# Kernel optimization log

Hardware: AMD Instinct MI355X
Metric: run time of the kernel (lower is better)

The kernel has to match this reference:

```python
import jax, jax.numpy as jnp
import numpy as np

B, S_IMG, S_TXT, P, D, HEADS, HD = 1, 2048, 512, 4, 3072, 24, 128


def rmsnorm(x, weight=None, eps=1e-6):
    var = jnp.mean(jnp.square(x), axis=-1, keepdims=True)
    y = x * jax.lax.rsqrt(var + eps)
    return y * weight if weight is not None else y


def apply_rope(x, cos, sin):
    # x: [B,H,S,Dh]; cos/sin: [S,Dh]; interleaved real/imag rotation (diffusers use_real_unbind_dim=-1)
    xr = x.reshape(*x.shape[:-1], -1, 2)
    rot = jnp.stack([-xr[..., 1], xr[..., 0]], axis=-1).reshape(x.shape)
    return x * cos[None, None] + rot * sin[None, None]


def sdpa(q, k, v):
    scores = jnp.einsum('bhqd,bhkd->bhqk', q, k) / jnp.sqrt(jnp.asarray(q.shape[-1], q.dtype))
    return jnp.einsum('bhqk,bhkd->bhqd', jax.nn.softmax(scores, axis=-1), v)


def heads_split(x):
    # [B,S,D] -> [B,H,S,Dh]
    return x.reshape(x.shape[0], x.shape[1], HEADS, HD).transpose(0, 2, 1, 3)


def heads_merge(x):
    # [B,H,S,Dh] -> [B,S,D]
    return x.transpose(0, 2, 1, 3).reshape(x.shape[0], x.shape[2], HEADS * HD)


def setup_inputs() -> dict:
    key = jax.random.key(0)
    ks = jax.random.split(key, 32)
    init = lambda k, shape: (jax.random.normal(k, shape, dtype=jnp.float32) * 0.02)
    inp = {
        'hidden_states': jax.random.normal(ks[0], (B, S_IMG, D), dtype=jnp.float32),
        'encoder_hidden_states': jax.random.normal(ks[1], (B, S_TXT, D), dtype=jnp.float32),
        'ip_encoder_hidden_states': jax.random.normal(ks[2], (B, P, D), dtype=jnp.float32),
        'layer_scale': jax.random.uniform(ks[3], (B,), dtype=jnp.float32),
        'Wq': init(ks[4], (D, D)), 'bq': jnp.zeros((D,), jnp.float32),
        'Wk': init(ks[5], (D, D)), 'bk': jnp.zeros((D,), jnp.float32),
        'Wv': init(ks[6], (D, D)), 'bv': jnp.zeros((D,), jnp.float32),
        'norm_q_w': jnp.ones((HD,), jnp.float32),
        'norm_k_w': jnp.ones((HD,), jnp.float32),
        'Waq': init(ks[7], (D, D)), 'baq': jnp.zeros((D,), jnp.float32),
        'Wak': init(ks[8], (D, D)), 'bak': jnp.zeros((D,), jnp.float32),
        'Wav': init(ks[9], (D, D)), 'bav': jnp.zeros((D,), jnp.float32),
        'norm_aq_w': jnp.ones((HD,), jnp.float32),
        'norm_ak_w': jnp.ones((HD,), jnp.float32),
        'Wk_ip': init(ks[10], (D, D)),
        'Wv_ip': init(ks[11], (D, D)),
        'Wo': init(ks[12], (D, D)), 'bo': jnp.zeros((D,), jnp.float32),
        'Wao': init(ks[13], (D, D)), 'bao': jnp.zeros((D,), jnp.float32),
    }
    # rotary cos/sin over the joint (text+image) sequence, interleaved freqs per diffusers FLUX
    pos = jnp.arange(S_TXT + S_IMG, dtype=jnp.float32)
    inv_freq = 1.0 / (10000.0 ** (jnp.arange(0, HD, 2, dtype=jnp.float32) / HD))
    angles = pos[:, None] * inv_freq[None, :]            # [S, HD/2]
    angles = jnp.repeat(angles, 2, axis=-1)              # [S, HD]
    inp['cos'] = jnp.cos(angles)
    inp['sin'] = jnp.sin(angles)
    return inp


IP_SCALE = 1.0  # self.scale


def reference(hidden_states, encoder_hidden_states, ip_encoder_hidden_states, cos, sin,
              layer_scale, Wq, bq, Wk, bk, Wv, bv, norm_q_w, norm_k_w,
              Waq, baq, Wak, bak, Wav, bav, norm_aq_w, norm_ak_w,
              Wk_ip, Wv_ip, Wo, bo, Wao, bao):
    # image-stream projections
    q = heads_split(hidden_states @ Wq.T + bq)
    k = heads_split(hidden_states @ Wk.T + bk)
    v = heads_split(hidden_states @ Wv.T + bv)
    q = rmsnorm(q, norm_q_w, 1e-6)
    k = rmsnorm(k, norm_k_w, 1e-6)

    # IP-adapter cross-attention (queries = image tokens, kv = IP tokens)
    ip_k = rmsnorm(heads_split(ip_encoder_hidden_states @ Wk_ip.T), None, 1e-5)
    ip_v = heads_split(ip_encoder_hidden_states @ Wv_ip.T)
    ip_out = heads_merge(sdpa(q, ip_k, ip_v))            # [B, S_img, D]

    # text (encoder) stream projections, prepended to joint sequence
    eq = rmsnorm(heads_split(encoder_hidden_states @ Waq.T + baq), norm_aq_w, 1e-6)
    ek = rmsnorm(heads_split(encoder_hidden_states @ Wak.T + bak), norm_ak_w, 1e-6)
    ev = heads_split(encoder_hidden_states @ Wav.T + bav)
    q = jnp.concatenate([eq, q], axis=2)
    k = jnp.concatenate([ek, k], axis=2)
    v = jnp.concatenate([ev, v], axis=2)

    q = apply_rope(q, cos, sin)
    k = apply_rope(k, cos, sin)

    out = heads_merge(sdpa(q, k, v))                     # [B, S_txt+S_img, D]
    n_txt = encoder_hidden_states.shape[1]
    enc_out, img_out = out[:, :n_txt], out[:, n_txt:]

    ls = layer_scale.reshape(-1, 1, 1)
    img_out = img_out + IP_SCALE * ls * ip_out
    img_out = img_out @ Wo.T + bo
    enc_out = enc_out @ Wao.T + bao
    return (img_out, enc_out)
```

## Files before the change

### kernel.cpp

```cpp
#include <hip/hip_runtime.h>

typedef _Float16 half_t;
typedef _Float16 half2v __attribute__((ext_vector_type(2)));
typedef _Float16 half4v __attribute__((ext_vector_type(4)));
typedef _Float16 half8v __attribute__((ext_vector_type(8)));
typedef float    float4v __attribute__((ext_vector_type(4)));
typedef short    short8v __attribute__((ext_vector_type(8)));

#define S_IMG 2048
#define S_TXT 512
#define S_TOT 2560
#define NH    24
#define HD    128
#define DM    3072

__device__ __forceinline__ void gload16(const void* g, void* l) {
  __builtin_amdgcn_global_load_lds(
      (const __attribute__((address_space(1))) unsigned int*)g,
      (__attribute__((address_space(3))) unsigned int*)l, 16, 0, 0);
}

__global__ void cvt_kernel(const float* __restrict__ s, half_t* __restrict__ d, int n) {
  int i = (blockIdx.x * 256 + threadIdx.x) * 4;
  int stride = gridDim.x * 256 * 4;
  for (; i < n; i += stride) {
    float4v v = *(const float4v*)(s + i);
    half4v h;
    h[0] = (half_t)v[0]; h[1] = (half_t)v[1]; h[2] = (half_t)v[2]; h[3] = (half_t)v[3];
    *(half4v*)(d + i) = h;
  }
}

__global__ void cvt3_kernel(const float* __restrict__ s0, const float* __restrict__ s1,
                            const float* __restrict__ s2,
                            half_t* __restrict__ d0, half_t* __restrict__ d1,
                            half_t* __restrict__ d2, int n) {
  const float* s = blockIdx.y == 0 ? s0 : (blockIdx.y == 1 ? s1 : s2);
  half_t* d = blockIdx.y == 0 ? d0 : (blockIdx.y == 1 ? d1 : d2);
  int i = (blockIdx.x * 256 + threadIdx.x) * 8;
  int stride = gridDim.x * 256 * 8;
  for (; i < n; i += stride) {
    float4v v0 = *(const float4v*)(s + i);
    float4v v1 = *(const float4v*)(s + i + 4);
    half8v h;
    h[0] = (half_t)v0[0]; h[1] = (half_t)v0[1]; h[2] = (half_t)v0[2]; h[3] = (half_t)v0[3];
    h[4] = (half_t)v1[0]; h[5] = (half_t)v1[1]; h[6] = (half_t)v1[2]; h[7] = (half_t)v1[3];
    *(half8v*)(d + i) = h;
  }
}

template <typename OUT>
__device__ __forceinline__ void gemm_tile(half_t* As, half_t* Bs,
                                          const half_t* __restrict__ A,
                                          const half_t* __restrict__ Bt,
                                          const float* __restrict__ bias,
                                          OUT* __restrict__ C, int bm, int bn) {
  const int K = DM, N = DM;
  const int tid = threadIdx.x, wid = tid >> 6, l = tid & 63;
  const int wm = (wid >> 1) * 64, wn = (wid & 1) * 64;
  const int l15 = l & 15, l4 = l >> 4;
  float4v acc[4][4] = {};

  const int scol = ((l & 3) ^ ((l >> 3) & 3)) * 8;
  const half_t* ga = A + (long)(bm + wid * 32 + (l >> 2)) * K + scol;
  const half_t* gb = Bt + (long)(bn + wid * 32 + (l >> 2)) * K + scol;
  const long rowstep = 16l * K;

#define GSTAGE(T, SEL)                                                        \
  {                                                                           \
    char* a_d = (char*)As + (SEL) * 8192 + wid * 2048;                        \
    char* b_d = (char*)Bs + (SEL) * 8192 + wid * 2048;                        \
    int k0 = (T) * 32;                                                        \
    gload16(ga + k0, a_d);                                                    \
    gload16(ga + rowstep + k0, a_d + 1024);                                   \
    gload16(gb + k0, b_d);                                                    \
    gload16(gb + rowstep + k0, b_d + 1024);                                   \
  }

  GSTAGE(0, 0);
  GSTAGE(1, 1);

  const int NT = K / 32;
  const int cofs = (l4 * 16) ^ (((l15 >> 1) & 3) << 4);
  for (int t = 0; t < NT; t++) {
    int cur = t % 3;
    if (t + 1 < NT) asm volatile("s_waitcnt vmcnt(4)" ::: "memory");
    else            asm volatile("s_waitcnt vmcnt(0)" ::: "memory");
    __builtin_amdgcn_s_barrier();
    __builtin_amdgcn_sched_barrier(0);
    if (t + 2 < NT) GSTAGE(t + 2, (t + 2) % 3);
    __builtin_amdgcn_sched_barrier(0);
    const char* AsB = (const char*)As + cur * 8192;
    const char* BsB = (const char*)Bs + cur * 8192;
    half8v af[4], bf[4];
#pragma unroll
    for (int i = 0; i < 4; i++)
      af[i] = *(const half8v*)(AsB + (wm + i * 16 + l15) * 64 + cofs);
#pragma unroll
    for (int j = 0; j < 4; j++)
      bf[j] = *(const half8v*)(BsB + (wn + j * 16 + l15) * 64 + cofs);
    __builtin_amdgcn_s_setprio(1);
#pragma unroll
    for (int i = 0; i < 4; i++)
#pragma unroll
      for (int j = 0; j < 4; j++)
        acc[i][j] = __builtin_amdgcn_mfma_f32_16x16x32_f16(af[i], bf[j], acc[i][j], 0, 0, 0);
    __builtin_amdgcn_s_setprio(0);
  }
#undef GSTAGE
#pragma unroll
  for (int i = 0; i < 4; i++)
#pragma unroll
    for (int j = 0; j < 4; j++) {
      int row = bm + wm + i * 16 + l4 * 4;
      int col = bn + wn + j * 16 + l15;
      float bv = bias ? bias[col] : 0.0f;
#pragma unroll
      for (int r = 0; r < 4; r++) {
        float v = acc[i][j][r] + bv;
        C[(long)(row + r) * N + col] = (OUT)v;
      }
    }
}

template <int NROW>
__global__ __launch_bounds__(256) void gemm3_kernel(const half_t* __restrict__ A,
                                                    const half_t* __restrict__ W0,
                                                    const half_t* __restrict__ W1,
                                                    const half_t* __restrict__ W2,
                                                    const float* b0, const float* b1, const float* b2,
                                                    half_t* O0, half_t* O1, half_t* O2) {
  __shared__ half_t As[3 * 128 * 32];
  __shared__ half_t Bs[3 * 128 * 32];
  int b = blockIdx.x;
  int q = (72 * NROW) >> 3;
  int wg = (b & 7) * q + (b >> 3);
  int col = wg / NROW, row = wg % NROW;
  int sel = col / 24;
  const half_t* Bt = sel == 0 ? W0 : (sel == 1 ? W1 : W2);
  const float* bias = sel == 0 ? b0 : (sel == 1 ? b1 : b2);
  half_t* C = sel == 0 ? O0 : (sel == 1 ? O1 : O2);
  gemm_tile<half_t>(As, Bs, A, Bt, bias, C, row * 128, (col % 24) * 128);
}

__global__ __launch_bounds__(256) void gemm_out_kernel(const half_t* __restrict__ ocomb,
                                                       const half_t* __restrict__ Wo_h,
                                                       const half_t* __restrict__ Wao_h,
                                                       const float* bo, const float* bao,
                                                       float* out_img, float* out_enc) {
  __shared__ half_t As[3 * 128 * 32];
  __shared__ half_t Bs[3 * 128 * 32];
  int b = blockIdx.x;
  int wg = (b & 7) * 60 + (b >> 3);
  int col = wg / 20, r = wg % 20;
  bool enc = r >= 16;
  const half_t* A = enc ? ocomb : ocomb + (long)S_TXT * DM;
  int bm = (enc ? (r - 16) : r) * 128;
  gemm_tile<float>(As, Bs, A, enc ? Wao_h : Wo_h, enc ? bao : bo,
                   enc ? out_enc : out_img, bm, col * 128);
}

__global__ __launch_bounds__(256) void ip_proj_kernel(const float* __restrict__ x,
                                                      const float* __restrict__ W,
                                                      float* __restrict__ out) {
  int n = blockIdx.x * 4 + (threadIdx.x >> 6);
  int l = threadIdx.x & 63;
  const float* wr = W + (long)n * DM;
  float acc[4] = {0.f, 0.f, 0.f, 0.f};
  for (int k = l * 4; k < DM; k += 256) {
    float4v wv = *(const float4v*)(wr + k);
#pragma unroll
    for (int p = 0; p < 4; p++) {
      float4v xv = *(const float4v*)(x + p * DM + k);
      acc[p] += wv[0] * xv[0] + wv[1] * xv[1] + wv[2] * xv[2] + wv[3] * xv[3];
    }
  }
#pragma unroll
  for (int off = 32; off; off >>= 1)
#pragma unroll
    for (int p = 0; p < 4; p++) acc[p] += __shfl_xor(acc[p], off, 64);
  if (l == 0)
#pragma unroll
    for (int p = 0; p < 4; p++) out[p * DM + n] = acc[p];
}

__global__ void ip_norm_kernel(const float* __restrict__ kr, const float* __restrict__ vr,
                               half_t* __restrict__ kh, half_t* __restrict__ vh) {
  int t = blockIdx.x;
  int l = threadIdx.x;
  int d = l * 2;
  if (t < 96) {
    int base = (t / 24) * DM + (t % 24) * HD;
    float x0 = kr[base + d], x1 = kr[base + d + 1];
    float ss = x0 * x0 + x1 * x1;
#pragma unroll
    for (int off = 32; off; off >>= 1) ss += __shfl_xor(ss, off, 64);
    float r = rsqrtf(ss * (1.0f / HD) + 1e-5f);
    kh[base + d] = (half_t)(x0 * r);
    kh[base + d + 1] = (half_t)(x1 * r);
  } else {
    int t2 = t - 96;
    int base = (t2 / 24) * DM + (t2 % 24) * HD;
    vh[base + d] = (half_t)vr[base + d];
    vh[base + d + 1] = (half_t)vr[base + d + 1];
  }
}

__global__ __launch_bounds__(256) void prep_kernel(
    const half_t* __restrict__ qraw, const half_t* __restrict__ kraw,
    const half_t* __restrict__ eq, const half_t* __restrict__ ek,
    const float* __restrict__ nqw, const float* __restrict__ nkw,
    const float* __restrict__ naqw, const float* __restrict__ nakw,
    const float* __restrict__ cosb, const float* __restrict__ sinb,
    half_t* __restrict__ qcat, half_t* __restrict__ kcat, half_t* __restrict__ qnr) {
  int task = blockIdx.x * 4 + (threadIdx.x >> 6);
  int l = threadIdx.x & 63;
  int s = task / NH, h = task - (task / NH) * NH;
  int d = l * 2;
  const half_t *qs, *ks;
  const float *wq, *wk;
  if (s < S_TXT) {
    long base = (long)s * DM + h * HD;
    qs = eq + base; ks = ek + base;
    wq = naqw; wk = nakw;
  } else {
    long base = (long)(s - S_TXT) * DM + h * HD;
    qs = qraw + base; ks = kraw + base;
    wq = nqw; wk = nkw;
  }
  half2v qv = *(const half2v*)(qs + d);
  half2v kv = *(const half2v*)(ks + d);
  float q0 = (float)qv[0], q1 = (float)qv[1];
  float k0 = (float)kv[0], k1 = (float)kv[1];
  float ssq = q0 * q0 + q1 * q1;
  float ssk = k0 * k0 + k1 * k1;
#pragma unroll
  for (int off = 32; off; off >>= 1) {
    ssq += __shfl_xor(ssq, off, 64);
    ssk += __shfl_xor(ssk, off, 64);
  }
  float rq = rsqrtf(ssq * (1.0f / HD) + 1e-6f);
  float rk = rsqrtf(ssk * (1.0f / HD) + 1e-6f);
  float qn0 = q0 * rq * wq[d], qn1 = q1 * rq * wq[d + 1];
  float kn0 = k0 * rk * wk[d], kn1 = k1 * rk * wk[d + 1];
  if (s >= S_TXT) {
    half2v o; o[0] = (half_t)qn0; o[1] = (half_t)qn1;
    *(half2v*)(qnr + ((long)h * S_IMG + (s - S_TXT)) * HD + d) = o;
  }
  float c0 = cosb[s * HD + d], c1 = cosb[s * HD + d + 1];
  float s0 = sinb[s * HD + d], s1 = sinb[s * HD + d + 1];
  float qo0 = qn0 * c0 - qn1 * s0, qo1 = qn1 * c1 + qn0 * s1;
  float ko0 = kn0 * c0 - kn1 * s0, ko1 = kn1 * c1 + kn0 * s1;
  long ci = ((long)h * S_TOT + s) * HD + d;
  half2v oq; oq[0] = (half_t)qo0; oq[1] = (half_t)qo1;
  half2v ok; ok[0] = (half_t)ko0; ok[1] = (half_t)ko1;
  *(half2v*)(qcat + ci) = oq;
  *(half2v*)(kcat + ci) = ok;
}

__global__ __launch_bounds__(256) void vtrans_kernel(const half_t* __restrict__ ev,
                                                     const half_t* __restrict__ vraw,
                                                     half_t* __restrict__ vcatT) {
  __shared__ half_t T[64][136];
  int h = blockIdx.y, sb = blockIdx.x * 64;
  int t = threadIdx.x;
#pragma unroll
  for (int i = 0; i < 4; i++) {
    int c = t + i * 256;
    int row = c >> 4, col = (c & 15) * 8;
    int s = sb + row;
    const half_t* src = (s < S_TXT) ? ev + (long)s * DM + h * HD + col
                                    : vraw + (long)(s - S_TXT) * DM + h * HD + col;
    *(half8v*)&T[row][col] = *(const half8v*)src;
  }
  __syncthreads();
#pragma unroll
  for (int i = 0; i < 4; i++) {
    int c = t + i * 256;
    int d = c >> 3, sc = (c & 7) * 8;
    half8v v;
#pragma unroll
    for (int j = 0; j < 8; j++) v[j] = T[sc + j][d];
    *(half8v*)(vcatT + ((long)h * HD + d) * S_TOT + sb + sc) = v;
  }
}

__global__ __launch_bounds__(256) void ip_attn_kernel(const half_t* __restrict__ qnr,
                                                      const half_t* __restrict__ kh,
                                                      const half_t* __restrict__ vh,
                                                      half_t* __restrict__ ipout) {
  int tid = threadIdx.x;
  int task = blockIdx.x * 16 + (tid >> 4);
  int l16 = tid & 15;
  int h = task >> 11;
  int s = task & 2047;
  int d = l16 * 8;
  half8v qv = *(const half8v*)(qnr + ((long)h * S_IMG + s) * HD + d);
  float sc[4];
#pragma unroll
  for (int p = 0; p < 4; p++) {
    half8v kv = *(const half8v*)(kh + p * DM + h * HD + d);
    float a = 0.f;
#pragma unroll
    for (int j = 0; j < 8; j++) a += (float)qv[j] * (float)kv[j];
    sc[p] = a;
  }
#pragma unroll
  for (int off = 8; off; off >>= 1)
#pragma unroll
    for (int p = 0; p < 4; p++) sc[p] += __shfl_xor(sc[p], off, 16);
  float m = fmaxf(fmaxf(sc[0], sc[1]), fmaxf(sc[2], sc[3]));
  float e[4], sum = 0.f;
#pragma unroll
  for (int p = 0; p < 4; p++) { e[p] = __expf((sc[p] - m) * 0.088388347648318447f); sum += e[p]; }
  float inv = 1.0f / sum;
  float o[8] = {};
#pragma unroll
  for (int p = 0; p < 4; p++) {
    half8v vv = *(const half8v*)(vh + p * DM + h * HD + d);
#pragma unroll
    for (int j = 0; j < 8; j++) o[j] += e[p] * (float)vv[j];
  }
  half8v ov;
#pragma unroll
  for (int j = 0; j < 8; j++) ov[j] = (half_t)(o[j] * inv);
  *(half8v*)(ipout + (long)s * DM + h * HD + d) = ov;
}

__global__ __launch_bounds__(256, 2) void flash_kernel(const half_t* __restrict__ qcat,
                                                       const half_t* __restrict__ kcat,
                                                       const half_t* __restrict__ vcatT,
                                                       const half_t* __restrict__ ipout,
                                                       const float* __restrict__ lsp,
                                                       half_t* __restrict__ ocomb) {
  __shared__ half_t Ks[3 * 32 * 128];
  __shared__ half_t Vs[3 * 128 * 32];
  __shared__ half_t Pw[4][32 * 40];
  int b = blockIdx.x;
  int wg = (b & 7) * 60 + (b >> 3);
  const int h = wg / 20, qb = wg % 20;
  const int tid = threadIdx.x, wid = tid >> 6, l = tid & 63;
  const int l15 = l & 15, l4 = l >> 4;
  const float CEXP = 0.12754137969983614f;

  half8v qf[2][4];
#pragma unroll
  for (int t = 0; t < 2; t++) {
    int qrow = qb * 128 + wid * 32 + t * 16 + l15;
    const half_t* qp = qcat + ((long)h * S_TOT + qrow) * HD;
#pragma unroll
    for (int kk = 0; kk < 4; kk++) qf[t][kk] = *(const half8v*)(qp + kk * 32 + l4 * 8);
  }
  float4v o[2][8] = {};
  float mreg[2] = {-3.0e38f, -3.0e38f};
  float lreg[2] = {0.f, 0.f};
  const float ls = lsp[0];

  const char* kb = (const char*)(kcat + (long)h * S_TOT * HD);
  const char* vb = (const char*)(vcatT + (long)h * HD * S_TOT);
  int kof[2];
  long vof[2];
#pragma unroll
  for (int c = 0; c < 2; c++) {
    int L = wid * 2048 + c * 1024 + l * 16;
    kof[c] = L ^ (((L >> 8) & 7) << 4);
    int vrow = L >> 6;
    vof[c] = (long)vrow * (S_TOT * 2) + ((L & 63) ^ (((vrow >> 1) & 3) << 4));
  }

#define STAGE(KT, SEL)                                                        \
  {                                                                           \
    char* kd = (char*)Ks + (SEL) * 8192 + wid * 2048;                         \
    char* vd = (char*)Vs + (SEL) * 8192 + wid * 2048;                         \
    _Pragma("unroll") for (int c = 0; c < 2; c++) {                           \
      gload16(kb + (long)(KT) * 256 + kof[c], kd + c * 1024);                 \
      gload16(vb + vof[c] + (KT) * 2, vd + c * 1024);                         \
    }                                                                         \
  }

  STAGE(0, 0);
  STAGE(32, 1);

  const int NT = S_TOT / 32;
  const int vofs = (l4 * 16) ^ (((l15 >> 1) & 3) << 4);
  for (int it = 0; it < NT; it++) {
    int cur = it % 3;
    if (it + 1 < NT) asm volatile("s_waitcnt vmcnt(4)" ::: "memory");
    else             asm volatile("s_waitcnt vmcnt(0)" ::: "memory");
    __builtin_amdgcn_s_barrier();
    __builtin_amdgcn_sched_barrier(0);
    if (it + 2 < NT) STAGE((it + 2) * 32, (it + 2) % 3);

    const char* KsB = (const char*)Ks + cur * 8192;
    const char* VsB = (const char*)Vs + cur * 8192;

    float4v s0[2] = {}, s1[2] = {};
    __builtin_amdgcn_s_setprio(1);
#pragma unroll
    for (int nb = 0; nb < 2; nb++) {
      int krow = nb * 16 + l15;
      int rb = krow << 8;
      int sw = (krow & 7) << 4;
#pragma unroll
      for (int kk = 0; kk < 4; kk++) {
        half8v kf = *(const half8v*)(KsB + rb + ((kk * 64 + l4 * 16) ^ sw));
        s0[nb] = __builtin_amdgcn_mfma_f32_16x16x32_f16(kf, qf[0][kk], s0[nb], 0, 0, 0);
        s1[nb] = __builtin_amdgcn_mfma_f32_16x16x32_f16(kf, qf[1][kk], s1[nb], 0, 0, 0);
      }
    }
    __builtin_amdgcn_s_setprio(0);
#pragma unroll
    for (int t = 0; t < 2; t++) {
      float4v* st = t ? s1 : s0;
      float mt = fmaxf(fmaxf(fmaxf(st[0][0], st[0][1]), fmaxf(st[0][2], st[0][3])),
                       fmaxf(fmaxf(st[1][0], st[1][1]), fmaxf(st[1][2], st[1][3])));
      mt = fmaxf(mt, __shfl_xor(mt, 16, 64));
      mt = fmaxf(mt, __shfl_xor(mt, 32, 64));
      if (__any((mt - mreg[t]) * CEXP > 8.0f)) {
        float mn = fmaxf(mreg[t], mt);
        float alv = exp2f((mreg[t] - mn) * CEXP);
        mreg[t] = mn;
        lreg[t] *= alv;
#pragma unroll
        for (int r = 0; r < 4; r++) {
          float ar = __shfl(alv, l4 * 4 + r, 64);
#pragma unroll
          for (int cb = 0; cb < 8; cb++) o[t][cb][r] *= ar;
        }
      }
      float sum = 0.f;
#pragma unroll
      for (int nb = 0; nb < 2; nb++) {
        half4v ph;
#pragma unroll
        for (int r = 0; r < 4; r++) {
          float e = exp2f((st[nb][r] - mreg[t]) * CEXP);
          sum += e;
          ph[r] = (half_t)e;
        }
        *(half4v*)&Pw[wid][(t * 16 + l15) * 40 + nb * 16 + l4 * 4] = ph;
      }
      sum += __shfl_xor(sum, 16, 64);
      sum += __shfl_xor(sum, 32, 64);
      lreg[t] += sum;
    }
    half8v pa0 = *(const half8v*)&Pw[wid][l15 * 40 + l4 * 8];
    half8v pa1 = *(const half8v*)&Pw[wid][(16 + l15) * 40 + l4 * 8];
    __builtin_amdgcn_s_setprio(1);
#pragma unroll
    for (int cb = 0; cb < 8; cb++) {
      int row = cb * 16 + l15;
      half8v vf = *(const half8v*)(VsB + row * 64 + vofs);
      o[0][cb] = __builtin_amdgcn_mfma_f32_16x16x32_f16(pa0, vf, o[0][cb], 0, 0, 0);
      o[1][cb] = __builtin_amdgcn_mfma_f32_16x16x32_f16(pa1, vf, o[1][cb], 0, 0, 0);
    }
    __builtin_amdgcn_s_setprio(0);
  }
#undef STAGE
#pragma unroll
  for (int t = 0; t < 2; t++) {
    float invq = 1.0f / lreg[t];
#pragma unroll
    for (int r = 0; r < 4; r++) {
      float inv = __shfl(invq, l4 * 4 + r, 64);
      int s = qb * 128 + wid * 32 + t * 16 + l4 * 4 + r;
#pragma unroll
      for (int cb = 0; cb < 8; cb++) {
        int col = h * HD + cb * 16 + l15;
        float val = o[t][cb][r] * inv;
        if (s >= S_TXT) val += ls * (float)ipout[(long)(s - S_TXT) * DM + col];
        ocomb[(long)s * DM + col] = (half_t)val;
      }
    }
  }
}

extern "C" void kernel_launch(void* const* d_in, const int* in_sizes, int n_in,
                              void* d_out, int out_size, void* d_ws, size_t ws_size,
                              hipStream_t stream) {
  (void)in_sizes; (void)n_in; (void)out_size; (void)ws_size;
  const float* hs    = (const float*)d_in[0];
  const float* enc   = (const float*)d_in[1];
  const float* ipenc = (const float*)d_in[2];
  const float* lsc   = (const float*)d_in[3];
  const float* Wq  = (const float*)d_in[4];  const float* bq  = (const float*)d_in[5];
  const float* Wk  = (const float*)d_in[6];  const float* bk  = (const float*)d_in[7];
  const float* Wv  = (const float*)d_in[8];  const float* bv  = (const float*)d_in[9];
  const float* nqw = (const float*)d_in[10]; const float* nkw = (const float*)d_in[11];
  const float* Waq = (const float*)d_in[12]; const float* baq = (const float*)d_in[13];
  const float* Wak = (const float*)d_in[14]; const float* bak = (const float*)d_in[15];
  const float* Wav = (const float*)d_in[16]; const float* bav = (const float*)d_in[17];
  const float* naqw= (const float*)d_in[18]; const float* nakw= (const float*)d_in[19];
  const float* Wkip= (const float*)d_in[20]; const float* Wvip= (const float*)d_in[21];
  const float* Wo  = (const float*)d_in[22]; const float* bo  = (const float*)d_in[23];
  const float* Wao = (const float*)d_in[24]; const float* bao = (const float*)d_in[25];
  const float* cosb= (const float*)d_in[26]; const float* sinb= (const float*)d_in[27];

  const size_t WSZ = (size_t)DM * DM;
  const size_t HSZ = (size_t)S_IMG * DM;
  const size_t ESZ = (size_t)S_TXT * DM;
  const size_t CSZ = (size_t)NH * S_TOT * HD;

  half_t* base = (half_t*)d_ws;
  half_t* W3    = base;
  half_t* hs_h  = W3 + 3 * WSZ;
  half_t* enc_h = hs_h + HSZ;
  half_t* qkvr  = enc_h + ESZ;
  half_t* eqkv  = qkvr + 3 * HSZ;
  half_t* qcat  = eqkv + 3 * ESZ;
  half_t* kcat  = qcat + CSZ;
  half_t* vcatT = kcat + CSZ;

  half_t* q_raw = qkvr;
  half_t* k_raw = qkvr + HSZ;
  half_t* v_raw = qkvr + 2 * HSZ;
  half_t* eq_r  = eqkv;
  half_t* ek_r  = eqkv + ESZ;
  half_t* ev_r  = eqkv + 2 * ESZ;
  half_t* qnr   = hs_h;
  half_t* ipout = qkvr;
  half_t* ocomb = qkvr + HSZ;
  float*  ipk_raw = (float*)enc_h;
  float*  ipv_raw = ipk_raw + 4 * DM;
  half_t* ipk_h  = enc_h + 16 * DM;
  half_t* ipv_h  = ipk_h + 4 * DM;

  cvt_kernel<<<1024, 256, 0, stream>>>(hs, hs_h, (int)HSZ);
  cvt_kernel<<<512, 256, 0, stream>>>(enc, enc_h, (int)ESZ);

  cvt3_kernel<<<dim3(1024, 3), 256, 0, stream>>>(Wq, Wk, Wv, W3, W3 + WSZ, W3 + 2 * WSZ, (int)WSZ);
  gemm3_kernel<16><<<1152, 256, 0, stream>>>(hs_h, W3, W3 + WSZ, W3 + 2 * WSZ,
                                             bq, bk, bv, q_raw, k_raw, v_raw);
  cvt3_kernel<<<dim3(1024, 3), 256, 0, stream>>>(Waq, Wak, Wav, W3, W3 + WSZ, W3 + 2 * WSZ, (int)WSZ);
  gemm3_kernel<4><<<288, 256, 0, stream>>>(enc_h, W3, W3 + WSZ, W3 + 2 * WSZ,
                                           baq, bak, bav, eq_r, ek_r, ev_r);
  ip_proj_kernel<<<768, 256, 0, stream>>>(ipenc, Wkip, ipk_raw);
  ip_proj_kernel<<<768, 256, 0, stream>>>(ipenc, Wvip, ipv_raw);
  ip_norm_kernel<<<192, 64, 0, stream>>>(ipk_raw, ipv_raw, ipk_h, ipv_h);

  prep_kernel<<<(S_TOT * NH) / 4, 256, 0, stream>>>(q_raw, k_raw, eq_r, ek_r,
                                                    nqw, nkw, naqw, nakw, cosb, sinb,
                                                    qcat, kcat, qnr);
  vtrans_kernel<<<dim3(S_TOT / 64, NH), 256, 0, stream>>>(ev_r, v_raw, vcatT);

  ip_attn_kernel<<<(NH * S_IMG) / 16, 256, 0, stream>>>(qnr, ipk_h, ipv_h, ipout);

  flash_kernel<<<480, 256, 0, stream>>>(qcat, kcat, vcatT, ipout, lsc, ocomb);

  float* out_img = (float*)d_out;
  float* out_enc = (float*)d_out + (size_t)S_IMG * DM;
  cvt3_kernel<<<dim3(1024, 2), 256, 0, stream>>>(Wo, Wao, Wao, W3, W3 + WSZ, W3 + 2 * WSZ, (int)WSZ);
  gemm_out_kernel<<<480, 256, 0, stream>>>(ocomb, W3, W3 + WSZ, bo, bao, out_img, out_enc);
}
```

Measured before the change: 600.0 us.

## Enlarge GEMM tiles to 128x256 with 8 waves, widen flash KV tile, merge launches

The GEMM tile grows to 128x256 with 512 threads (8 waves), which halves the grid and raises B-tile reuse per A load. The flash attention kernel now processes 64-key tiles with double buffering instead of 32-key triple buffering, and does the PV MFMA per query sub-tile. The activation conversions and the two IP projections are each merged into a single launch. The larger tiles reduce the number of workgroups, and the change of buffering may expose load latency or lower occupancy.

Result: slower. 642.7 us (+7.1%).

```diff
diff --git a/kernel.cpp b/kernel.cpp
--- a/kernel.cpp
+++ b/kernel.cpp
@@ -20,14 +20,20 @@
       (__attribute__((address_space(3))) unsigned int*)l, 16, 0, 0);
 }
 
-__global__ void cvt_kernel(const float* __restrict__ s, half_t* __restrict__ d, int n) {
-  int i = (blockIdx.x * 256 + threadIdx.x) * 4;
-  int stride = gridDim.x * 256 * 4;
-  for (; i < n; i += stride) {
-    float4v v = *(const float4v*)(s + i);
-    half4v h;
-    h[0] = (half_t)v[0]; h[1] = (half_t)v[1]; h[2] = (half_t)v[2]; h[3] = (half_t)v[3];
-    *(half4v*)(d + i) = h;
+__global__ void cvt_act_kernel(const float* __restrict__ hs, const float* __restrict__ enc,
+                               half_t* __restrict__ d) {
+  const long NHS = (long)S_IMG * DM;
+  const long TOT = NHS + (long)S_TXT * DM;
+  long i = ((long)blockIdx.x * 256 + threadIdx.x) * 8;
+  long stride = (long)gridDim.x * 256 * 8;
+  for (; i < TOT; i += stride) {
+    const float* s = i < NHS ? hs + i : enc + (i - NHS);
+    float4v v0 = *(const float4v*)(s);
+    float4v v1 = *(const float4v*)(s + 4);
+    half8v h;
+    h[0] = (half_t)v0[0]; h[1] = (half_t)v0[1]; h[2] = (half_t)v0[2]; h[3] = (half_t)v0[3];
+    h[4] = (half_t)v1[0]; h[5] = (half_t)v1[1]; h[6] = (half_t)v1[2]; h[7] = (half_t)v1[3];
+    *(half8v*)(d + i) = h;
   }
 }
 
@@ -57,24 +63,23 @@
                                           OUT* __restrict__ C, int bm, int bn) {
   const int K = DM, N = DM;
   const int tid = threadIdx.x, wid = tid >> 6, l = tid & 63;
-  const int wm = (wid >> 1) * 64, wn = (wid & 1) * 64;
+  const int wm = (wid >> 2) * 64, wn = (wid & 3) * 64;
   const int l15 = l & 15, l4 = l >> 4;
   float4v acc[4][4] = {};
 
-  const int scol = ((l & 3) ^ ((l >> 3) & 3)) * 8;
-  const half_t* ga = A + (long)(bm + wid * 32 + (l >> 2)) * K + scol;
-  const half_t* gb = Bt + (long)(bn + wid * 32 + (l >> 2)) * K + scol;
-  const long rowstep = 16l * K;
+  const int scol = ((tid & 3) ^ ((tid >> 3) & 3)) * 8;
+  const half_t* ga = A + (long)(bm + (tid >> 2)) * K + scol;
+  const half_t* gb = Bt + (long)(bn + (tid >> 2)) * K + scol;
+  const long rowstepB = 128l * K;
 
 #define GSTAGE(T, SEL)                                                        \
   {                                                                           \
-    char* a_d = (char*)As + (SEL) * 8192 + wid * 2048;                        \
-    char* b_d = (char*)Bs + (SEL) * 8192 + wid * 2048;                        \
+    char* a_d = (char*)As + (SEL) * 8192 + wid * 1024;                        \
+    char* b_d = (char*)Bs + (SEL) * 16384 + wid * 1024;                       \
     int k0 = (T) * 32;                                                        \
     gload16(ga + k0, a_d);                                                    \
-    gload16(ga + rowstep + k0, a_d + 1024);                                   \
     gload16(gb + k0, b_d);                                                    \
-    gload16(gb + rowstep + k0, b_d + 1024);                                   \
+    gload16(gb + rowstepB + k0, b_d + 8192);                                  \
   }
 
   GSTAGE(0, 0);
@@ -84,14 +89,14 @@
   const int cofs = (l4 * 16) ^ (((l15 >> 1) & 3) << 4);
   for (int t = 0; t < NT; t++) {
     int cur = t % 3;
-    if (t + 1 < NT) asm volatile("s_waitcnt vmcnt(4)" ::: "memory");
+    if (t + 1 < NT) asm volatile("s_waitcnt vmcnt(3)" ::: "memory");
     else            asm volatile("s_waitcnt vmcnt(0)" ::: "memory");
     __builtin_amdgcn_s_barrier();
     __builtin_amdgcn_sched_barrier(0);
     if (t + 2 < NT) GSTAGE(t + 2, (t + 2) % 3);
     __builtin_amdgcn_sched_barrier(0);
     const char* AsB = (const char*)As + cur * 8192;
-    const char* BsB = (const char*)Bs + cur * 8192;
+    const char* BsB = (const char*)Bs + cur * 16384;
     half8v af[4], bf[4];
 #pragma unroll
     for (int i = 0; i < 4; i++)
@@ -124,45 +129,49 @@
 }
 
 template <int NROW>
-__global__ __launch_bounds__(256) void gemm3_kernel(const half_t* __restrict__ A,
-                                                    const half_t* __restrict__ W0,
-                                                    const half_t* __restrict__ W1,
-                                                    const half_t* __restrict__ W2,
-                                                    const float* b0, const float* b1, const float* b2,
-                                                    half_t* O0, half_t* O1, half_t* O2) {
-  __shared__ half_t As[3 * 128 * 32];
-  __shared__ half_t Bs[3 * 128 * 32];
+__global__ __launch_bounds__(512, 4) void gemm3_kernel(const half_t* __restrict__ A,
+                                                       const half_t* __restrict__ W0,
+                                                       const half_t* __restrict__ W1,
+                                                       const half_t* __restrict__ W2,
+                                                       const float* b0, const float* b1, const float* b2,
+                                                       half_t* O0, half_t* O1, half_t* O2) {
+  __shared__ half_t As[3 * 4096];
+  __shared__ half_t Bs[3 * 8192];
   int b = blockIdx.x;
-  int q = (72 * NROW) >> 3;
+  int q = (36 * NROW) >> 3;
   int wg = (b & 7) * q + (b >> 3);
   int col = wg / NROW, row = wg % NROW;
-  int sel = col / 24;
+  int sel = col / 12;
   const half_t* Bt = sel == 0 ? W0 : (sel == 1 ? W1 : W2);
   const float* bias = sel == 0 ? b0 : (sel == 1 ? b1 : b2);
   half_t* C = sel == 0 ? O0 : (sel == 1 ? O1 : O2);
-  gemm_tile<half_t>(As, Bs, A, Bt, bias, C, row * 128, (col % 24) * 128);
-}
-
-__global__ __launch_bounds__(256) void gemm_out_kernel(const half_t* __restrict__ ocomb,
-                                                       const half_t* __restrict__ Wo_h,
-                                                       const half_t* __restrict__ Wao_h,
-                                                       const float* bo, const float* bao,
-                                                       float* out_img, float* out_enc) {
-  __shared__ half_t As[3 * 128 * 32];
-  __shared__ half_t Bs[3 * 128 * 32];
+  gemm_tile<half_t>(As, Bs, A, Bt, bias, C, row * 128, (col % 12) * 256);
+}
+
+__global__ __launch_bounds__(512, 4) void gemm_out_kernel(const half_t* __restrict__ ocomb,
+                                                          const half_t* __restrict__ Wo_h,
+                                                          const half_t* __restrict__ Wao_h,
+                                                          const float* bo, const float* bao,
+                                                          float* out_img, float* out_enc) {
+  __shared__ half_t As[3 * 4096];
+  __shared__ half_t Bs[3 * 8192];
   int b = blockIdx.x;
-  int wg = (b & 7) * 60 + (b >> 3);
+  int wg = (b & 7) * 30 + (b >> 3);
   int col = wg / 20, r = wg % 20;
   bool enc = r >= 16;
   const half_t* A = enc ? ocomb : ocomb + (long)S_TXT * DM;
   int bm = (enc ? (r - 16) : r) * 128;
   gemm_tile<float>(As, Bs, A, enc ? Wao_h : Wo_h, enc ? bao : bo,
-                   enc ? out_enc : out_img, bm, col * 128);
+                   enc ? out_enc : out_img, bm, col * 256);
 }
 
 __global__ __launch_bounds__(256) void ip_proj_kernel(const float* __restrict__ x,
-                                                      const float* __restrict__ W,
-                                                      float* __restrict__ out) {
+                                                      const float* __restrict__ Wk_ip,
+                                                      const float* __restrict__ Wv_ip,
+                                                      float* __restrict__ outk,
+                                                      float* __restrict__ outv) {
+  const float* W = blockIdx.y ? Wv_ip : Wk_ip;
+  float* out = blockIdx.y ? outv : outk;
   int n = blockIdx.x * 4 + (threadIdx.x >> 6);
   int l = threadIdx.x & 63;
   const float* wr = W + (long)n * DM;
@@ -333,9 +342,9 @@
                                                        const half_t* __restrict__ ipout,
                                                        const float* __restrict__ lsp,
                                                        half_t* __restrict__ ocomb) {
-  __shared__ half_t Ks[3 * 32 * 128];
-  __shared__ half_t Vs[3 * 128 * 32];
-  __shared__ half_t Pw[4][32 * 40];
+  __shared__ half_t Ks[2 * 64 * 128];
+  __shared__ half_t Vs[2 * 128 * 64];
+  __shared__ half_t Pw[4][16 * 72];
   int b = blockIdx.x;
   int wg = (b & 7) * 60 + (b >> 3);
   const int h = wg / 20, qb = wg % 20;
@@ -358,46 +367,43 @@
 
   const char* kb = (const char*)(kcat + (long)h * S_TOT * HD);
   const char* vb = (const char*)(vcatT + (long)h * HD * S_TOT);
-  int kof[2];
-  long vof[2];
-#pragma unroll
-  for (int c = 0; c < 2; c++) {
-    int L = wid * 2048 + c * 1024 + l * 16;
+  int kof[4];
+  long vof[4];
+#pragma unroll
+  for (int c = 0; c < 4; c++) {
+    int L = c * 4096 + tid * 16;
     kof[c] = L ^ (((L >> 8) & 7) << 4);
-    int vrow = L >> 6;
-    vof[c] = (long)vrow * (S_TOT * 2) + ((L & 63) ^ (((vrow >> 1) & 3) << 4));
+    int vrow = L >> 7;
+    vof[c] = (long)vrow * (S_TOT * 2) + ((L & 127) ^ ((vrow & 7) << 4));
   }
 
 #define STAGE(KT, SEL)                                                        \
   {                                                                           \
-    char* kd = (char*)Ks + (SEL) * 8192 + wid * 2048;                         \
-    char* vd = (char*)Vs + (SEL) * 8192 + wid * 2048;                         \
-    _Pragma("unroll") for (int c = 0; c < 2; c++) {                           \
-      gload16(kb + (long)(KT) * 256 + kof[c], kd + c * 1024);                 \
-      gload16(vb + vof[c] + (KT) * 2, vd + c * 1024);                         \
+    char* kd = (char*)Ks + (SEL) * 16384 + wid * 1024;                        \
+    char* vd = (char*)Vs + (SEL) * 16384 + wid * 1024;                        \
+    _Pragma("unroll") for (int c = 0; c < 4; c++) {                           \
+      gload16(kb + (long)(KT) * 256 + kof[c], kd + c * 4096);                 \
+      gload16(vb + vof[c] + (KT) * 2, vd + c * 4096);                         \
     }                                                                         \
   }
 
   STAGE(0, 0);
-  STAGE(32, 1);
-
-  const int NT = S_TOT / 32;
-  const int vofs = (l4 * 16) ^ (((l15 >> 1) & 3) << 4);
+
+  const int NT = S_TOT / 64;
+  int sel = 0;
   for (int it = 0; it < NT; it++) {
-    int cur = it % 3;
-    if (it + 1 < NT) asm volatile("s_waitcnt vmcnt(4)" ::: "memory");
-    else             asm volatile("s_waitcnt vmcnt(0)" ::: "memory");
+    asm volatile("s_waitcnt vmcnt(0)" ::: "memory");
     __builtin_amdgcn_s_barrier();
     __builtin_amdgcn_sched_barrier(0);
-    if (it + 2 < NT) STAGE((it + 2) * 32, (it + 2) % 3);
-
-    const char* KsB = (const char*)Ks + cur * 8192;
-    const char* VsB = (const char*)Vs + cur * 8192;
-
-    float4v s0[2] = {}, s1[2] = {};
+    if (it + 1 < NT) STAGE((it + 1) * 64, sel ^ 1);
+
+    const char* KsB = (const char*)Ks + sel * 16384;
+    const char* VsB = (const char*)Vs + sel * 16384;
+
+    float4v s0[4] = {}, s1[4] = {};
     __builtin_amdgcn_s_setprio(1);
 #pragma unroll
-    for (int nb = 0; nb < 2; nb++) {
+    for (int nb = 0; nb < 4; nb++) {
       int krow = nb * 16 + l15;
       int rb = krow << 8;
       int sw = (krow & 7) << 4;
@@ -414,6 +420,8 @@
       float4v* st = t ? s1 : s0;
       float mt = fmaxf(fmaxf(fmaxf(st[0][0], st[0][1]), fmaxf(st[0][2], st[0][3])),
                        fmaxf(fmaxf(st[1][0], st[1][1]), fmaxf(st[1][2], st[1][3])));
+      mt = fmaxf(mt, fmaxf(fmaxf(fmaxf(st[2][0], st[2][1]), fmaxf(st[2][2], st[2][3])),
+                           fmaxf(fmaxf(st[3][0], st[3][1]), fmaxf(st[3][2], st[3][3]))));
       mt = fmaxf(mt, __shfl_xor(mt, 16, 64));
       mt = fmaxf(mt, __shfl_xor(mt, 32, 64));
       if (__any((mt - mreg[t]) * CEXP > 8.0f)) {
@@ -430,7 +438,7 @@
       }
       float sum = 0.f;
 #pragma unroll
-      for (int nb = 0; nb < 2; nb++) {
+      for (int nb = 0; nb < 4; nb++) {
         half4v ph;
 #pragma unroll
         for (int r = 0; r < 4; r++) {
@@ -438,23 +446,26 @@
           sum += e;
           ph[r] = (half_t)e;
         }
-        *(half4v*)&Pw[wid][(t * 16 + l15) * 40 + nb * 16 + l4 * 4] = ph;
+        *(half4v*)&Pw[wid][l15 * 72 + nb * 16 + l4 * 4] = ph;
       }
       sum += __shfl_xor(sum, 16, 64);
       sum += __shfl_xor(sum, 32, 64);
       lreg[t] += sum;
+      half8v pa0 = *(const half8v*)&Pw[wid][l15 * 72 + l4 * 8];
+      half8v pa1 = *(const half8v*)&Pw[wid][l15 * 72 + 32 + l4 * 8];
+      __builtin_amdgcn_s_setprio(1);
+#pragma unroll
+      for (int cb = 0; cb < 8; cb++) {
+        int row = cb * 16 + l15;
+        int sw = (row & 7) << 4;
+        half8v vf0 = *(const half8v*)(VsB + (row << 7) + ((l4 * 16) ^ sw));
+        half8v vf1 = *(const half8v*)(VsB + (row << 7) + ((64 + l4 * 16) ^ sw));
+        o[t][cb] = __builtin_amdgcn_mfma_f32_16x16x32_f16(pa0, vf0, o[t][cb], 0, 0, 0);
+        o[t][cb] = __builtin_amdgcn_mfma_f32_16x16x32_f16(pa1, vf1, o[t][cb], 0, 0, 0);
+      }
+      __builtin_amdgcn_s_setprio(0);
     }
-    half8v pa0 = *(const half8v*)&Pw[wid][l15 * 40 + l4 * 8];
-    half8v pa1 = *(const half8v*)&Pw[wid][(16 + l15) * 40 + l4 * 8];
-    __builtin_amdgcn_s_setprio(1);
-#pragma unroll
-    for (int cb = 0; cb < 8; cb++) {
-      int row = cb * 16 + l15;
-      half8v vf = *(const half8v*)(VsB + row * 64 + vofs);
-      o[0][cb] = __builtin_amdgcn_mfma_f32_16x16x32_f16(pa0, vf, o[0][cb], 0, 0, 0);
-      o[1][cb] = __builtin_amdgcn_mfma_f32_16x16x32_f16(pa1, vf, o[1][cb], 0, 0, 0);
-    }
-    __builtin_amdgcn_s_setprio(0);
+    sel ^= 1;
   }
 #undef STAGE
 #pragma unroll
@@ -525,17 +536,15 @@
   half_t* ipk_h  = enc_h + 16 * DM;
   half_t* ipv_h  = ipk_h + 4 * DM;
 
-  cvt_kernel<<<1024, 256, 0, stream>>>(hs, hs_h, (int)HSZ);
-  cvt_kernel<<<512, 256, 0, stream>>>(enc, enc_h, (int)ESZ);
+  cvt_act_kernel<<<2048, 256, 0, stream>>>(hs, enc, hs_h);
 
   cvt3_kernel<<<dim3(1024, 3), 256, 0, stream>>>(Wq, Wk, Wv, W3, W3 + WSZ, W3 + 2 * WSZ, (int)WSZ);
-  gemm3_kernel<16><<<1152, 256, 0, stream>>>(hs_h, W3, W3 + WSZ, W3 + 2 * WSZ,
-                                             bq, bk, bv, q_raw, k_raw, v_raw);
+  gemm3_kernel<16><<<576, 512, 0, stream>>>(hs_h, W3, W3 + WSZ, W3 + 2 * WSZ,
+                                            bq, bk, bv, q_raw, k_raw, v_raw);
   cvt3_kernel<<<dim3(1024, 3), 256, 0, stream>>>(Waq, Wak, Wav, W3, W3 + WSZ, W3 + 2 * WSZ, (int)WSZ);
-  gemm3_kernel<4><<<288, 256, 0, stream>>>(enc_h, W3, W3 + WSZ, W3 + 2 * WSZ,
+  gemm3_kernel<4><<<144, 512, 0, stream>>>(enc_h, W3, W3 + WSZ, W3 + 2 * WSZ,
                                            baq, bak, bav, eq_r, ek_r, ev_r);
-  ip_proj_kernel<<<768, 256, 0, stream>>>(ipenc, Wkip, ipk_raw);
-  ip_proj_kernel<<<768, 256, 0, stream>>>(ipenc, Wvip, ipv_raw);
+  ip_proj_kernel<<<dim3(768, 2), 256, 0, stream>>>(ipenc, Wkip, Wvip, ipk_raw, ipv_raw);
   ip_norm_kernel<<<192, 64, 0, stream>>>(ipk_raw, ipv_raw, ipk_h, ipv_h);
 
   prep_kernel<<<(S_TOT * NH) / 4, 256, 0, stream>>>(q_raw, k_raw, eq_r, ek_r,
@@ -550,5 +559,5 @@
   float* out_img = (float*)d_out;
   float* out_enc = (float*)d_out + (size_t)S_IMG * DM;
   cvt3_kernel<<<dim3(1024, 2), 256, 0, stream>>>(Wo, Wao, Wao, W3, W3 + WSZ, W3 + 2 * WSZ, (int)WSZ);
-  gemm_out_kernel<<<480, 256, 0, stream>>>(ocomb, W3, W3 + WSZ, bo, bao, out_img, out_enc);
-}
+  gemm_out_kernel<<<240, 512, 0, stream>>>(ocomb, W3, W3 + WSZ, bo, bao, out_img, out_enc);
+}
```
